# Kernel optimization log

Measured on AMD Instinct MI355X. Metric: run time of the kernel, lower is better.

The kernel has to match this reference:

```python
import jax, jax.numpy as jnp
import numpy as np

NUM_EXPERTS = 8
N_EMBD = 1024
D_FF = 4 * N_EMBD
B, S = 4, 2048


def setup_inputs() -> dict:
    key = jax.random.key(0)
    ks = jax.random.split(key, 6)
    x = jax.random.normal(ks[0], (B, S, N_EMBD), dtype=jnp.float32)
    gate_w = jax.random.normal(ks[1], (N_EMBD, NUM_EXPERTS), dtype=jnp.float32) * 0.02
    w1 = jax.random.normal(ks[2], (NUM_EXPERTS, N_EMBD, D_FF), dtype=jnp.float32) * 0.02
    b1 = jnp.zeros((NUM_EXPERTS, D_FF), dtype=jnp.float32)
    w2 = jax.random.normal(ks[3], (NUM_EXPERTS, D_FF, N_EMBD), dtype=jnp.float32) * 0.02
    b2 = jnp.zeros((NUM_EXPERTS, N_EMBD), dtype=jnp.float32)
    return {"x": x, "gate_w": gate_w, "w1": w1, "b1": b1, "w2": w2, "b2": b2}


def reference(x, gate_w, w1, b1, w2, b2):
    Bb, Ss, D = x.shape
    x_flat = x.reshape(-1, D)                      # [T, D]
    router_logits = x_flat @ gate_w                # [T, E]
    router_probs = jax.nn.softmax(router_logits, axis=-1)
    expert_idx = jnp.argmax(router_probs, axis=-1)             # [T] int
    expert_w = jnp.take_along_axis(router_probs, expert_idx[:, None], axis=1)[:, 0]  # [T]

    out = jnp.zeros_like(x_flat)
    # fixed small loop over experts (structurally distinct weights)
    for e in range(NUM_EXPERTS):
        h = jax.nn.gelu(x_flat @ w1[e] + b1[e], approximate=False)  # [T, 4D]
        y = h @ w2[e] + b2[e]                                        # [T, D]
        sel = (expert_idx == e)
        out = out + jnp.where(sel, expert_w, 0.0)[:, None] * y
    return out.reshape(Bb, Ss, D)
```

## Files before the change

### kernel.cpp

```cpp
#include <hip/hip_runtime.h>
#include <math.h>
#include <stdint.h>

#define T_TOK  8192
#define DMODEL 1024
#define DFF    4096
#define NEXP   8

static constexpr size_t OFF_COUNTS  = 0;
static constexpr size_t OFF_CURSOR  = 64;
static constexpr size_t OFF_OFFSETS = 128;
static constexpr size_t OFF_EIDX    = 1024;
static constexpr size_t OFF_EW      = OFF_EIDX + (size_t)T_TOK * 4;
static constexpr size_t OFF_PERM    = OFF_EW   + (size_t)T_TOK * 4;
static constexpr size_t OFF_XB      = 131072;
static constexpr size_t OFF_W1B     = OFF_XB  + (size_t)T_TOK * DMODEL * 2;
static constexpr size_t OFF_W2B     = OFF_W1B + (size_t)NEXP * DFF * DMODEL * 2;
static constexpr size_t OFF_HB      = OFF_W2B + (size_t)NEXP * DMODEL * DFF * 2;

typedef __attribute__((ext_vector_type(8))) short short8;
typedef __attribute__((ext_vector_type(4))) float floatx4;

__device__ __forceinline__ unsigned short f2bf(float f) {
    unsigned u = __builtin_bit_cast(unsigned, f);
    u += 0x7fffu + ((u >> 16) & 1u);
    return (unsigned short)(u >> 16);
}

__device__ __forceinline__ void async16(const unsigned short* g, unsigned short* l) {
    __builtin_amdgcn_global_load_lds(
        (const __attribute__((address_space(1))) unsigned*)g,
        (__attribute__((address_space(3))) unsigned*)l, 16, 0, 0);
}

__global__ void zero_kernel(int* counts, int* cursor) {
    int t = threadIdx.x;
    if (t < NEXP) { counts[t] = 0; cursor[t] = 0; }
}

__global__ __launch_bounds__(256) void convert_x_kernel(const float* __restrict__ x,
                                                        unsigned short* __restrict__ xb) {
    int i = (blockIdx.x * 256 + threadIdx.x) * 4;
    float4 v = *(const float4*)(x + i);
    unsigned a = (unsigned)f2bf(v.x) | ((unsigned)f2bf(v.y) << 16);
    unsigned b = (unsigned)f2bf(v.z) | ((unsigned)f2bf(v.w) << 16);
    uint2 p; p.x = a; p.y = b;
    *(uint2*)(xb + i) = p;
}

__global__ __launch_bounds__(256) void transpose_cvt_kernel(const float* __restrict__ src,
                                                            unsigned short* __restrict__ dst,
                                                            int K, int N) {
    int e  = blockIdx.z;
    int k0 = blockIdx.x * 64;
    int n0 = blockIdx.y * 64;
    const float* s = src + (size_t)e * K * N;
    unsigned short* d = dst + (size_t)e * K * N;
    __shared__ float tile[64][65];
    int tid = threadIdx.x;
    int col = tid & 63, rb = tid >> 6;
#pragma unroll
    for (int i = 0; i < 16; i++) {
        int row = i * 4 + rb;
        tile[row][col] = s[(size_t)(k0 + row) * N + n0 + col];
    }
    __syncthreads();
    int kk = (tid & 31) * 2, nb = tid >> 5;
#pragma unroll
    for (int i = 0; i < 8; i++) {
        int n = i * 8 + nb;
        unsigned a = f2bf(tile[kk][n]);
        unsigned b = f2bf(tile[kk + 1][n]);
        *(unsigned*)(d + (size_t)(n0 + n) * K + k0 + kk) = a | (b << 16);
    }
}

__global__ __launch_bounds__(256) void router_kernel(const float* __restrict__ x,
                                                     const float* __restrict__ gw,
                                                     int* __restrict__ eidx,
                                                     float* __restrict__ ew) {
    int tid = threadIdx.x, lane = tid & 63, w = tid >> 6;
    int t = blockIdx.x * 4 + w;
    float acc[NEXP];
#pragma unroll
    for (int e = 0; e < NEXP; e++) acc[e] = 0.f;
    const float* xr = x + (size_t)t * DMODEL;
#pragma unroll
    for (int i = 0; i < 4; i++) {
        int dbase = i * 256 + lane * 4;
        float4 xv = *(const float4*)(xr + dbase);
        float xs[4] = {xv.x, xv.y, xv.z, xv.w};
#pragma unroll
        for (int j = 0; j < 4; j++) {
            const float* gr = gw + (size_t)(dbase + j) * NEXP;
            float4 g0 = *(const float4*)(gr);
            float4 g1 = *(const float4*)(gr + 4);
            acc[0] += xs[j] * g0.x; acc[1] += xs[j] * g0.y;
            acc[2] += xs[j] * g0.z; acc[3] += xs[j] * g0.w;
            acc[4] += xs[j] * g1.x; acc[5] += xs[j] * g1.y;
            acc[6] += xs[j] * g1.z; acc[7] += xs[j] * g1.w;
        }
    }
#pragma unroll
    for (int e = 0; e < NEXP; e++) {
#pragma unroll
        for (int o = 32; o > 0; o >>= 1) acc[e] += __shfl_xor(acc[e], o, 64);
    }
    float m = acc[0]; int a = 0;
#pragma unroll
    for (int e = 1; e < NEXP; e++) { if (acc[e] > m) { m = acc[e]; a = e; } }
    float s = 0.f;
#pragma unroll
    for (int e = 0; e < NEXP; e++) s += expf(acc[e] - m);
    if (lane == 0) { eidx[t] = a; ew[t] = 1.0f / s; }
}

__global__ void hist_kernel(const int* __restrict__ eidx, int* __restrict__ counts) {
    __shared__ int lh[NEXP];
    int tid = threadIdx.x;
    if (tid < NEXP) lh[tid] = 0;
    __syncthreads();
    int e = eidx[blockIdx.x * 256 + tid];
    atomicAdd(&lh[e], 1);
    __syncthreads();
    if (tid < NEXP) atomicAdd(&counts[tid], lh[tid]);
}

__global__ void scan_kernel(const int* __restrict__ counts, int* __restrict__ offsets,
                            int* __restrict__ cursor) {
    if (threadIdx.x == 0) {
        int s = 0;
        for (int e = 0; e < NEXP; e++) { offsets[e] = s; cursor[e] = s; s += counts[e]; }
        offsets[NEXP] = s;
    }
}

__global__ void scatter_kernel(const int* __restrict__ eidx, int* __restrict__ cursor,
                               int* __restrict__ perm) {
    __shared__ int lh[NEXP];
    __shared__ int lbase[NEXP];
    int tid = threadIdx.x;
    if (tid < NEXP) lh[tid] = 0;
    __syncthreads();
    int t = blockIdx.x * 256 + tid;
    int e = eidx[t];
    int lpos = atomicAdd(&lh[e], 1);
    __syncthreads();
    if (tid < NEXP) lbase[tid] = atomicAdd(&cursor[tid], lh[tid]);
    __syncthreads();
    perm[lbase[e] + lpos] = t;
}

__global__ __launch_bounds__(256, 2) void gemm1_kernel(
    const unsigned short* __restrict__ xb,
    const unsigned short* __restrict__ w1b,
    const float* __restrict__ b1,
    const int* __restrict__ counts,
    const int* __restrict__ offsets,
    const int* __restrict__ perm,
    unsigned short* __restrict__ hb)
{
    const int e = blockIdx.z, mt = blockIdx.y, nt = blockIdx.x;
    const int cnt = counts[e];
    if (mt * 128 >= cnt) return;
    const int off = offsets[e];
    const int tid = threadIdx.x, lane = tid & 63, wave = tid >> 6;
    const int wm = (wave >> 1) * 64, wn = (wave & 1) * 64;
    const int lm = lane & 15, quad = lane >> 4;

    __shared__ __attribute__((aligned(16))) unsigned short As[128 * 64];
    __shared__ __attribute__((aligned(16))) unsigned short Bs[128 * 64];

    const unsigned short* a_src[4];
    const unsigned short* b_src[4];
    const int cntLoc = cnt - mt * 128;
#pragma unroll
    for (int i = 0; i < 4; i++) {
        int c = i * 256 + tid;
        int row = c >> 3;
        int g = (c & 7) ^ (row & 7);
        int r = (row < cntLoc) ? row : 0;
        int tok = perm[off + mt * 128 + r];
        a_src[i] = xb + (size_t)tok * DMODEL + g * 8;
        b_src[i] = w1b + ((size_t)e * DFF + nt * 128 + row) * DMODEL + g * 8;
    }

    floatx4 acc[4][4];
#pragma unroll
    for (int i = 0; i < 4; i++)
#pragma unroll
        for (int j = 0; j < 4; j++) acc[i][j] = floatx4{0.f, 0.f, 0.f, 0.f};

    for (int k0 = 0; k0 < DMODEL; k0 += 64) {
#pragma unroll
        for (int i = 0; i < 4; i++) {
            async16(a_src[i] + k0, &As[(i * 256 + tid) * 8]);
            async16(b_src[i] + k0, &Bs[(i * 256 + tid) * 8]);
        }
        __syncthreads();
#pragma unroll
        for (int kk = 0; kk < 2; kk++) {
            short8 af[4], bfr[4];
#pragma unroll
            for (int im = 0; im < 4; im++) {
                int m = wm + im * 16 + lm;
                int slot = (kk * 4 + quad) ^ (m & 7);
                af[im] = *(const short8*)(&As[m * 64 + slot * 8]);
            }
#pragma unroll
            for (int in = 0; in < 4; in++) {
                int n = wn + in * 16 + lm;
                int slot = (kk * 4 + quad) ^ (n & 7);
                bfr[in] = *(const short8*)(&Bs[n * 64 + slot * 8]);
            }
#pragma unroll
            for (int im = 0; im < 4; im++)
#pragma unroll
                for (int in = 0; in < 4; in++)
                    acc[im][in] = __builtin_amdgcn_mfma_f32_16x16x32_bf16(
                        af[im], bfr[in], acc[im][in], 0, 0, 0);
        }
        __syncthreads();
    }

    float b1v[4];
#pragma unroll
    for (int in = 0; in < 4; in++) b1v[in] = b1[e * DFF + nt * 128 + wn + in * 16 + lm];
#pragma unroll
    for (int im = 0; im < 4; im++) {
#pragma unroll
        for (int r = 0; r < 4; r++) {
            int row = mt * 128 + wm + im * 16 + quad * 4 + r;
            if (row < cnt) {
                size_t base = (size_t)(off + row) * DFF + nt * 128 + wn + lm;
#pragma unroll
                for (int in = 0; in < 4; in++) {
                    float v = acc[im][in][r] + b1v[in];
                    float gl = 0.5f * v * (1.0f + erff(v * 0.7071067811865475f));
                    hb[base + in * 16] = f2bf(gl);
                }
            }
        }
    }
}

__global__ __launch_bounds__(256, 2) void gemm2_kernel(
    const unsigned short* __restrict__ hb,
    const unsigned short* __restrict__ w2b,
    const float* __restrict__ b2,
    const int* __restrict__ counts,
    const int* __restrict__ offsets,
    const int* __restrict__ perm,
    const float* __restrict__ ew,
    float* __restrict__ out)
{
    const int e = blockIdx.z, mt = blockIdx.y, nt = blockIdx.x;
    const int cnt = counts[e];
    if (mt * 128 >= cnt) return;
    const int off = offsets[e];
    const int tid = threadIdx.x, lane = tid & 63, wave = tid >> 6;
    const int wm = (wave >> 1) * 64, wn = (wave & 1) * 64;
    const int lm = lane & 15, quad = lane >> 4;

    __shared__ __attribute__((aligned(16))) unsigned short As[128 * 64];
    __shared__ __attribute__((aligned(16))) unsigned short Bs[128 * 64];

    const unsigned short* a_src[4];
    const unsigned short* b_src[4];
#pragma unroll
    for (int i = 0; i < 4; i++) {
        int c = i * 256 + tid;
        int row = c >> 3;
        int g = (c & 7) ^ (row & 7);
        int gr = off + mt * 128 + row;
        if (gr > T_TOK - 1) gr = T_TOK - 1;
        a_src[i] = hb + (size_t)gr * DFF + g * 8;
        b_src[i] = w2b + ((size_t)e * DMODEL + nt * 128 + row) * DFF + g * 8;
    }

    floatx4 acc[4][4];
#pragma unroll
    for (int i = 0; i < 4; i++)
#pragma unroll
        for (int j = 0; j < 4; j++) acc[i][j] = floatx4{0.f, 0.f, 0.f, 0.f};

    for (int k0 = 0; k0 < DFF; k0 += 64) {
#pragma unroll
        for (int i = 0; i < 4; i++) {
            async16(a_src[i] + k0, &As[(i * 256 + tid) * 8]);
            async16(b_src[i] + k0, &Bs[(i * 256 + tid) * 8]);
        }
        __syncthreads();
#pragma unroll
        for (int kk = 0; kk < 2; kk++) {
            short8 af[4], bfr[4];
#pragma unroll
            for (int im = 0; im < 4; im++) {
                int m = wm + im * 16 + lm;
                int slot = (kk * 4 + quad) ^ (m & 7);
                af[im] = *(const short8*)(&As[m * 64 + slot * 8]);
            }
#pragma unroll
            for (int in = 0; in < 4; in++) {
                int n = wn + in * 16 + lm;
                int slot = (kk * 4 + quad) ^ (n & 7);
                bfr[in] = *(const short8*)(&Bs[n * 64 + slot * 8]);
            }
#pragma unroll
            for (int im = 0; im < 4; im++)
#pragma unroll
                for (int in = 0; in < 4; in++)
                    acc[im][in] = __builtin_amdgcn_mfma_f32_16x16x32_bf16(
                        af[im], bfr[in], acc[im][in], 0, 0, 0);
        }
        __syncthreads();
    }

    float b2v[4];
#pragma unroll
    for (int in = 0; in < 4; in++) b2v[in] = b2[e * DMODEL + nt * 128 + wn + in * 16 + lm];
#pragma unroll
    for (int im = 0; im < 4; im++) {
#pragma unroll
        for (int r = 0; r < 4; r++) {
            int row = mt * 128 + wm + im * 16 + quad * 4 + r;
            if (row < cnt) {
                int tok = perm[off + row];
                float wv = ew[tok];
                size_t base = (size_t)tok * DMODEL + nt * 128 + wn + lm;
#pragma unroll
                for (int in = 0; in < 4; in++)
                    out[base + in * 16] = (acc[im][in][r] + b2v[in]) * wv;
            }
        }
    }
}

extern "C" void kernel_launch(void* const* d_in, const int* in_sizes, int n_in,
                              void* d_out, int out_size, void* d_ws, size_t ws_size,
                              hipStream_t stream) {
    const float* x      = (const float*)d_in[0];
    const float* gate_w = (const float*)d_in[1];
    const float* w1     = (const float*)d_in[2];
    const float* b1     = (const float*)d_in[3];
    const float* w2     = (const float*)d_in[4];
    const float* b2     = (const float*)d_in[5];
    float* out = (float*)d_out;
    char* ws = (char*)d_ws;

    int* counts  = (int*)(ws + OFF_COUNTS);
    int* cursor  = (int*)(ws + OFF_CURSOR);
    int* offsets = (int*)(ws + OFF_OFFSETS);
    int* eidx    = (int*)(ws + OFF_EIDX);
    float* ew    = (float*)(ws + OFF_EW);
    int* perm    = (int*)(ws + OFF_PERM);
    unsigned short* xb  = (unsigned short*)(ws + OFF_XB);
    unsigned short* w1b = (unsigned short*)(ws + OFF_W1B);
    unsigned short* w2b = (unsigned short*)(ws + OFF_W2B);
    unsigned short* hb  = (unsigned short*)(ws + OFF_HB);

    zero_kernel<<<1, 64, 0, stream>>>(counts, cursor);
    convert_x_kernel<<<(T_TOK * DMODEL) / (256 * 4), 256, 0, stream>>>(x, xb);
    {
        dim3 g(DMODEL / 64, DFF / 64, NEXP);
        transpose_cvt_kernel<<<g, 256, 0, stream>>>(w1, w1b, DMODEL, DFF);
    }
    {
        dim3 g(DFF / 64, DMODEL / 64, NEXP);
        transpose_cvt_kernel<<<g, 256, 0, stream>>>(w2, w2b, DFF, DMODEL);
    }
    router_kernel<<<T_TOK / 4, 256, 0, stream>>>(x, gate_w, eidx, ew);
    hist_kernel<<<T_TOK / 256, 256, 0, stream>>>(eidx, counts);
    scan_kernel<<<1, 64, 0, stream>>>(counts, offsets, cursor);
    scatter_kernel<<<T_TOK / 256, 256, 0, stream>>>(eidx, cursor, perm);
    {
        dim3 g(DFF / 128, T_TOK / 128, NEXP);
        gemm1_kernel<<<g, 256, 0, stream>>>(xb, w1b, b1, counts, offsets, perm, hb);
    }
    {
        dim3 g(DMODEL / 128, T_TOK / 128, NEXP);
        gemm2_kernel<<<g, 256, 0, stream>>>(hb, w2b, b2, counts, offsets, perm, ew, out);
    }
}
```

Baseline: 605.8 us.

## Compact expert tile grid, split-K gemm2 with atomics, fuse x conversion into router

```diff
diff --git a/kernel.cpp b/kernel.cpp
--- a/kernel.cpp
+++ b/kernel.cpp
@@ -6,10 +6,14 @@
 #define DMODEL 1024
 #define DFF    4096
 #define NEXP   8
+#define MAXTILES 71
+#define KSPLIT 4
 
 static constexpr size_t OFF_COUNTS  = 0;
 static constexpr size_t OFF_CURSOR  = 64;
 static constexpr size_t OFF_OFFSETS = 128;
+static constexpr size_t OFF_TILES   = 256;
+static constexpr size_t OFF_NTILES  = 768;
 static constexpr size_t OFF_EIDX    = 1024;
 static constexpr size_t OFF_EW      = OFF_EIDX + (size_t)T_TOK * 4;
 static constexpr size_t OFF_PERM    = OFF_EW   + (size_t)T_TOK * 4;
@@ -36,16 +40,6 @@
 __global__ void zero_kernel(int* counts, int* cursor) {
     int t = threadIdx.x;
     if (t < NEXP) { counts[t] = 0; cursor[t] = 0; }
-}
-
-__global__ __launch_bounds__(256) void convert_x_kernel(const float* __restrict__ x,
-                                                        unsigned short* __restrict__ xb) {
-    int i = (blockIdx.x * 256 + threadIdx.x) * 4;
-    float4 v = *(const float4*)(x + i);
-    unsigned a = (unsigned)f2bf(v.x) | ((unsigned)f2bf(v.y) << 16);
-    unsigned b = (unsigned)f2bf(v.z) | ((unsigned)f2bf(v.w) << 16);
-    uint2 p; p.x = a; p.y = b;
-    *(uint2*)(xb + i) = p;
 }
 
 __global__ __launch_bounds__(256) void transpose_cvt_kernel(const float* __restrict__ src,
@@ -58,37 +52,52 @@
     unsigned short* d = dst + (size_t)e * K * N;
     __shared__ float tile[64][65];
     int tid = threadIdx.x;
-    int col = tid & 63, rb = tid >> 6;
-#pragma unroll
-    for (int i = 0; i < 16; i++) {
-        int row = i * 4 + rb;
-        tile[row][col] = s[(size_t)(k0 + row) * N + n0 + col];
-    }
-    __syncthreads();
-    int kk = (tid & 31) * 2, nb = tid >> 5;
-#pragma unroll
-    for (int i = 0; i < 8; i++) {
-        int n = i * 8 + nb;
-        unsigned a = f2bf(tile[kk][n]);
-        unsigned b = f2bf(tile[kk + 1][n]);
-        *(unsigned*)(d + (size_t)(n0 + n) * K + k0 + kk) = a | (b << 16);
+    int lane16 = tid & 15, rowb = tid >> 4;
+#pragma unroll
+    for (int i = 0; i < 4; i++) {
+        int row = i * 16 + rowb;
+        float4 v = *(const float4*)(s + (size_t)(k0 + row) * N + n0 + lane16 * 4);
+        tile[row][lane16 * 4 + 0] = v.x;
+        tile[row][lane16 * 4 + 1] = v.y;
+        tile[row][lane16 * 4 + 2] = v.z;
+        tile[row][lane16 * 4 + 3] = v.w;
+    }
+    __syncthreads();
+    int n = tid >> 2, kq = tid & 3;
+#pragma unroll
+    for (int h = 0; h < 2; h++) {
+        int kk = (kq + h * 4) * 8;
+        unsigned pk[4];
+#pragma unroll
+        for (int j = 0; j < 4; j++) {
+            unsigned lo = f2bf(tile[kk + 2 * j][n]);
+            unsigned hi = f2bf(tile[kk + 2 * j + 1][n]);
+            pk[j] = lo | (hi << 16);
+        }
+        *(uint4*)(d + (size_t)(n0 + n) * K + k0 + kk) = *(uint4*)pk;
     }
 }
 
 __global__ __launch_bounds__(256) void router_kernel(const float* __restrict__ x,
                                                      const float* __restrict__ gw,
                                                      int* __restrict__ eidx,
-                                                     float* __restrict__ ew) {
+                                                     float* __restrict__ ew,
+                                                     unsigned short* __restrict__ xb) {
     int tid = threadIdx.x, lane = tid & 63, w = tid >> 6;
     int t = blockIdx.x * 4 + w;
     float acc[NEXP];
 #pragma unroll
     for (int e = 0; e < NEXP; e++) acc[e] = 0.f;
     const float* xr = x + (size_t)t * DMODEL;
+    unsigned short* xbr = xb + (size_t)t * DMODEL;
 #pragma unroll
     for (int i = 0; i < 4; i++) {
         int dbase = i * 256 + lane * 4;
         float4 xv = *(const float4*)(xr + dbase);
+        uint2 p;
+        p.x = (unsigned)f2bf(xv.x) | ((unsigned)f2bf(xv.y) << 16);
+        p.y = (unsigned)f2bf(xv.z) | ((unsigned)f2bf(xv.w) << 16);
+        *(uint2*)(xbr + dbase) = p;
         float xs[4] = {xv.x, xv.y, xv.z, xv.w};
 #pragma unroll
         for (int j = 0; j < 4; j++) {
@@ -127,11 +136,19 @@
 }
 
 __global__ void scan_kernel(const int* __restrict__ counts, int* __restrict__ offsets,
-                            int* __restrict__ cursor) {
+                            int* __restrict__ cursor, int* __restrict__ tiletab,
+                            int* __restrict__ ntiles) {
     if (threadIdx.x == 0) {
-        int s = 0;
-        for (int e = 0; e < NEXP; e++) { offsets[e] = s; cursor[e] = s; s += counts[e]; }
+        int s = 0, nt = 0;
+        for (int e = 0; e < NEXP; e++) {
+            offsets[e] = s; cursor[e] = s;
+            int c = counts[e];
+            int m = (c + 127) >> 7;
+            for (int i = 0; i < m; i++) tiletab[nt++] = (e << 16) | i;
+            s += c;
+        }
         offsets[NEXP] = s;
+        ntiles[0] = nt;
     }
 }
 
@@ -158,11 +175,15 @@
     const int* __restrict__ counts,
     const int* __restrict__ offsets,
     const int* __restrict__ perm,
+    const int* __restrict__ tiletab,
+    const int* __restrict__ ntiles,
     unsigned short* __restrict__ hb)
 {
-    const int e = blockIdx.z, mt = blockIdx.y, nt = blockIdx.x;
+    const int ti = blockIdx.y;
+    if (ti >= ntiles[0]) return;
+    const int tv = tiletab[ti];
+    const int e = tv >> 16, mt = tv & 0xffff, nt = blockIdx.x;
     const int cnt = counts[e];
-    if (mt * 128 >= cnt) return;
     const int off = offsets[e];
     const int tid = threadIdx.x, lane = tid & 63, wave = tid >> 6;
     const int wm = (wave >> 1) * 64, wn = (wave & 1) * 64;
@@ -251,16 +272,22 @@
     const int* __restrict__ counts,
     const int* __restrict__ offsets,
     const int* __restrict__ perm,
+    const int* __restrict__ tiletab,
+    const int* __restrict__ ntiles,
     const float* __restrict__ ew,
     float* __restrict__ out)
 {
-    const int e = blockIdx.z, mt = blockIdx.y, nt = blockIdx.x;
+    const int ti = blockIdx.y;
+    if (ti >= ntiles[0]) return;
+    const int tv = tiletab[ti];
+    const int e = tv >> 16, mt = tv & 0xffff, nt = blockIdx.x, slice = blockIdx.z;
     const int cnt = counts[e];
-    if (mt * 128 >= cnt) return;
     const int off = offsets[e];
     const int tid = threadIdx.x, lane = tid & 63, wave = tid >> 6;
     const int wm = (wave >> 1) * 64, wn = (wave & 1) * 64;
     const int lm = lane & 15, quad = lane >> 4;
+    const int kbeg = slice * (DFF / KSPLIT);
+    const int kend = kbeg + (DFF / KSPLIT);
 
     __shared__ __attribute__((aligned(16))) unsigned short As[128 * 64];
     __shared__ __attribute__((aligned(16))) unsigned short Bs[128 * 64];
@@ -284,7 +311,7 @@
 #pragma unroll
         for (int j = 0; j < 4; j++) acc[i][j] = floatx4{0.f, 0.f, 0.f, 0.f};
 
-    for (int k0 = 0; k0 < DFF; k0 += 64) {
+    for (int k0 = kbeg; k0 < kend; k0 += 64) {
 #pragma unroll
         for (int i = 0; i < 4; i++) {
             async16(a_src[i] + k0, &As[(i * 256 + tid) * 8]);
@@ -318,7 +345,8 @@
 
     float b2v[4];
 #pragma unroll
-    for (int in = 0; in < 4; in++) b2v[in] = b2[e * DMODEL + nt * 128 + wn + in * 16 + lm];
+    for (int in = 0; in < 4; in++)
+        b2v[in] = (slice == 0) ? b2[e * DMODEL + nt * 128 + wn + in * 16 + lm] : 0.f;
 #pragma unroll
     for (int im = 0; im < 4; im++) {
 #pragma unroll
@@ -330,7 +358,7 @@
                 size_t base = (size_t)tok * DMODEL + nt * 128 + wn + lm;
 #pragma unroll
                 for (int in = 0; in < 4; in++)
-                    out[base + in * 16] = (acc[im][in][r] + b2v[in]) * wv;
+                    atomicAdd(&out[base + in * 16], (acc[im][in][r] + b2v[in]) * wv);
             }
         }
     }
@@ -351,6 +379,8 @@
     int* counts  = (int*)(ws + OFF_COUNTS);
     int* cursor  = (int*)(ws + OFF_CURSOR);
     int* offsets = (int*)(ws + OFF_OFFSETS);
+    int* tiletab = (int*)(ws + OFF_TILES);
+    int* ntiles  = (int*)(ws + OFF_NTILES);
     int* eidx    = (int*)(ws + OFF_EIDX);
     float* ew    = (float*)(ws + OFF_EW);
     int* perm    = (int*)(ws + OFF_PERM);
@@ -359,8 +389,8 @@
     unsigned short* w2b = (unsigned short*)(ws + OFF_W2B);
     unsigned short* hb  = (unsigned short*)(ws + OFF_HB);
 
+    hipMemsetAsync(out, 0, (size_t)out_size * sizeof(float), stream);
     zero_kernel<<<1, 64, 0, stream>>>(counts, cursor);
-    convert_x_kernel<<<(T_TOK * DMODEL) / (256 * 4), 256, 0, stream>>>(x, xb);
     {
         dim3 g(DMODEL / 64, DFF / 64, NEXP);
         transpose_cvt_kernel<<<g, 256, 0, stream>>>(w1, w1b, DMODEL, DFF);
@@ -369,16 +399,18 @@
         dim3 g(DFF / 64, DMODEL / 64, NEXP);
         transpose_cvt_kernel<<<g, 256, 0, stream>>>(w2, w2b, DFF, DMODEL);
     }
-    router_kernel<<<T_TOK / 4, 256, 0, stream>>>(x, gate_w, eidx, ew);
+    router_kernel<<<T_TOK / 4, 256, 0, stream>>>(x, gate_w, eidx, ew, xb);
     hist_kernel<<<T_TOK / 256, 256, 0, stream>>>(eidx, counts);
-    scan_kernel<<<1, 64, 0, stream>>>(counts, offsets, cursor);
+    scan_kernel<<<1, 64, 0, stream>>>(counts, offsets, cursor, tiletab, ntiles);
     scatter_kernel<<<T_TOK / 256, 256, 0, stream>>>(eidx, cursor, perm);
     {
-        dim3 g(DFF / 128, T_TOK / 128, NEXP);
-        gemm1_kernel<<<g, 256, 0, stream>>>(xb, w1b, b1, counts, offsets, perm, hb);
+        dim3 g(DFF / 128, MAXTILES);
+        gemm1_kernel<<<g, 256, 0, stream>>>(xb, w1b, b1, counts, offsets, perm,
+                                            tiletab, ntiles, hb);
     }
     {
-        dim3 g(DMODEL / 128, T_TOK / 128, NEXP);
-        gemm2_kernel<<<g, 256, 0, stream>>>(hb, w2b, b2, counts, offsets, perm, ew, out);
-    }
-}
+        dim3 g(DMODEL / 128, MAXTILES, KSPLIT);
+        gemm2_kernel<<<g, 256, 0, stream>>>(hb, w2b, b2, counts, offsets, perm,
+                                            tiletab, ntiles, ew, out);
+    }
+}
```

Result: slower. 650.6 us (+7.4%).
